# Kernel optimization log

Measured on AMD Instinct MI355X. Metric: run time of the kernel, lower is better.

## Reference

```python
import jax, jax.numpy as jnp
import numpy as np

GN_EPS = 1e-5
NUM_GROUPS = 32


def setup_inputs() -> dict:
    key = jax.random.key(0)
    ks = jax.random.split(key, 4)
    B, K, N = 8192, 2048, 4096
    bound = 1.0 / np.sqrt(K)
    return {
        "x": jax.random.normal(ks[0], (B, K), dtype=jnp.float32),
        "weight": jax.random.normal(ks[1], (N, K), dtype=jnp.float32) * bound,
        "bias_lin": jax.random.uniform(ks[2], (N,), dtype=jnp.float32, minval=-bound, maxval=bound),
        "bias_extra": jax.random.normal(ks[3], (N,), dtype=jnp.float32),
        "gn_weight": jnp.ones((N,), dtype=jnp.float32),
        "gn_bias": jnp.zeros((N,), dtype=jnp.float32),
    }


def reference(x, weight, bias_lin, bias_extra, gn_weight, gn_bias):
    # Fused GEMM + bias + Swish + extra bias:  y = swish(x @ W.T + b_lin) + b_ex
    z = jnp.einsum("bk,nk->bn", x, weight) + bias_lin          # [B, N]
    y = z * jax.nn.sigmoid(z) + bias_extra                      # Swish + extra bias
    # GroupNorm over channel groups
    B, N = y.shape
    G = NUM_GROUPS
    yg = y.reshape(B, G, N // G)
    mean = jnp.mean(yg, axis=2, keepdims=True)
    var = jnp.mean(jnp.square(yg - mean), axis=2, keepdims=True)  # biased variance
    y_norm = ((yg - mean) * jax.lax.rsqrt(var + GN_EPS)).reshape(B, N)
    return y_norm * gn_weight + gn_bias
```

## Files before the change

### kernel.cpp

```cpp
#include <hip/hip_runtime.h>


typedef __attribute__((ext_vector_type(8))) short short8;
typedef __attribute__((ext_vector_type(4))) float f32x4;

#define M_DIM 8192
#define N_DIM 4096
#define K_DIM 2048
#define BM 256
#define BN 256
#define BK 64
#define NT (K_DIM / BK)

__global__ void f32_to_bf16_k(const float* __restrict__ in, ushort* __restrict__ out, int n8) {
    int i = blockIdx.x * blockDim.x + threadIdx.x;
    if (i >= n8) return;
    const float4* p = (const float4*)in + 2 * (size_t)i;
    float4 a = p[0], b = p[1];
    float v[8] = {a.x, a.y, a.z, a.w, b.x, b.y, b.z, b.w};
    ushort rr[8];
#pragma unroll
    for (int j = 0; j < 8; ++j) {
        unsigned u = __float_as_uint(v[j]);
        rr[j] = (ushort)((u + 0x7fffu + ((u >> 16) & 1u)) >> 16);
    }
    uint4 o;
    o.x = (unsigned)rr[0] | ((unsigned)rr[1] << 16);
    o.y = (unsigned)rr[2] | ((unsigned)rr[3] << 16);
    o.z = (unsigned)rr[4] | ((unsigned)rr[5] << 16);
    o.w = (unsigned)rr[6] | ((unsigned)rr[7] << 16);
    ((uint4*)out)[i] = o;
}

__global__ __launch_bounds__(512, 2) void gemm_swish_gn(
    const ushort* __restrict__ xb, const ushort* __restrict__ wb,
    const float* __restrict__ bias_lin, const float* __restrict__ bias_extra,
    const float* __restrict__ gn_w, const float* __restrict__ gn_b,
    float* __restrict__ out)
{
    extern __shared__ __align__(16) ushort lds[];

    const int t = threadIdx.x;
    const int w = t >> 6;
    const int l = t & 63;
    const int wm = w >> 2;
    const int wn = w & 3;
    const int h = l >> 4;
    const int r = l & 15;

    const int bid = blockIdx.x;
    const int id = (bid & 7) * 64 + (bid >> 3);
    const int brow = id & 31;
    const int bcol = id >> 5;

    const int strow = t >> 3;
    const int scb = (t & 7) << 4;
    const int scbs = scb ^ ((strow & 7) << 4);
    const ushort* srcA[4];
    const ushort* srcB[4];
#pragma unroll
    for (int rd = 0; rd < 4; ++rd) {
        srcA[rd] = xb + (size_t)(brow * BM + rd * 64 + strow) * K_DIM + (scbs >> 1);
        srcB[rd] = wb + (size_t)(bcol * BN + rd * 64 + strow) * K_DIM + (scbs >> 1);
    }
    const int dstoff = t * 8;

#define STAGE(buf_) do {                                                          \
    _Pragma("unroll")                                                             \
    for (int rd = 0; rd < 4; ++rd) {                                              \
        __builtin_amdgcn_global_load_lds(                                         \
            (const __attribute__((address_space(1))) void*)srcA[rd],              \
            (__attribute__((address_space(3))) void*)&lds[((buf_)*2+0)*16384 + rd*4096 + dstoff], \
            16, 0, 0);                                                            \
        srcA[rd] += BK;                                                           \
    }                                                                             \
    _Pragma("unroll")                                                             \
    for (int rd = 0; rd < 4; ++rd) {                                              \
        __builtin_amdgcn_global_load_lds(                                         \
            (const __attribute__((address_space(1))) void*)srcB[rd],              \
            (__attribute__((address_space(3))) void*)&lds[((buf_)*2+1)*16384 + rd*4096 + dstoff], \
            16, 0, 0);                                                            \
        srcB[rd] += BK;                                                           \
    }                                                                             \
} while (0)

    f32x4 acc[8][4];
#pragma unroll
    for (int m = 0; m < 8; ++m)
#pragma unroll
        for (int n = 0; n < 4; ++n)
            acc[m][n] = f32x4{0.f, 0.f, 0.f, 0.f};

    STAGE(0);
    STAGE(1);

    const int xr = (r & 7) << 4;
    const int aBase = wm * 128 + r;
    const int bBase = wn * 64 + r;

    short8 aF[8], bF[8];

#pragma unroll 1
    for (int tt = 0; tt < NT; ++tt) {
        if (tt < NT - 1) asm volatile("s_waitcnt vmcnt(8)" ::: "memory");
        else             asm volatile("s_waitcnt vmcnt(0)" ::: "memory");
        __builtin_amdgcn_sched_barrier(0);
        __builtin_amdgcn_s_barrier();
        __builtin_amdgcn_sched_barrier(0);

        const int cur = tt & 1;
        const ushort* sA = &lds[(cur * 2 + 0) * 16384];
        const ushort* sB = &lds[(cur * 2 + 1) * 16384];

#pragma unroll
        for (int m = 0; m < 4; ++m)
#pragma unroll
            for (int kk = 0; kk < 2; ++kk) {
                int row = aBase + m * 16;
                aF[m * 2 + kk] = *(const short8*)&sA[(row * 128 + ((kk * 64 + h * 16) ^ xr)) >> 1];
            }
#pragma unroll
        for (int n = 0; n < 2; ++n)
#pragma unroll
            for (int kk = 0; kk < 2; ++kk) {
                int row = bBase + n * 16;
                bF[n * 2 + kk] = *(const short8*)&sB[(row * 128 + ((kk * 64 + h * 16) ^ xr)) >> 1];
            }
        __builtin_amdgcn_s_setprio(1);
#pragma unroll
        for (int m = 0; m < 4; ++m)
#pragma unroll
            for (int n = 0; n < 2; ++n)
#pragma unroll
                for (int kk = 0; kk < 2; ++kk)
                    acc[m][n] = __builtin_amdgcn_mfma_f32_16x16x32_bf16(aF[m * 2 + kk], bF[n * 2 + kk], acc[m][n], 0, 0, 0);
        __builtin_amdgcn_s_setprio(0);

#pragma unroll
        for (int n = 2; n < 4; ++n)
#pragma unroll
            for (int kk = 0; kk < 2; ++kk) {
                int row = bBase + n * 16;
                bF[n * 2 + kk] = *(const short8*)&sB[(row * 128 + ((kk * 64 + h * 16) ^ xr)) >> 1];
            }
        __builtin_amdgcn_s_setprio(1);
#pragma unroll
        for (int m = 0; m < 4; ++m)
#pragma unroll
            for (int n = 2; n < 4; ++n)
#pragma unroll
                for (int kk = 0; kk < 2; ++kk)
                    acc[m][n] = __builtin_amdgcn_mfma_f32_16x16x32_bf16(aF[m * 2 + kk], bF[n * 2 + kk], acc[m][n], 0, 0, 0);
        __builtin_amdgcn_s_setprio(0);

#pragma unroll
        for (int m = 4; m < 8; ++m)
#pragma unroll
            for (int kk = 0; kk < 2; ++kk) {
                int row = aBase + m * 16;
                aF[(m - 4) * 2 + kk] = *(const short8*)&sA[(row * 128 + ((kk * 64 + h * 16) ^ xr)) >> 1];
            }
        __builtin_amdgcn_s_setprio(1);
#pragma unroll
        for (int m = 4; m < 8; ++m)
#pragma unroll
            for (int n = 2; n < 4; ++n)
#pragma unroll
                for (int kk = 0; kk < 2; ++kk)
                    acc[m][n] = __builtin_amdgcn_mfma_f32_16x16x32_bf16(aF[(m - 4) * 2 + kk], bF[n * 2 + kk], acc[m][n], 0, 0, 0);
        __builtin_amdgcn_s_setprio(0);

        __builtin_amdgcn_s_barrier();
        if (tt + 2 < NT) STAGE(tt & 1);

        __builtin_amdgcn_s_setprio(1);
#pragma unroll
        for (int m = 4; m < 8; ++m)
#pragma unroll
            for (int n = 0; n < 2; ++n)
#pragma unroll
                for (int kk = 0; kk < 2; ++kk)
                    acc[m][n] = __builtin_amdgcn_mfma_f32_16x16x32_bf16(aF[(m - 4) * 2 + kk], bF[n * 2 + kk], acc[m][n], 0, 0, 0);
        __builtin_amdgcn_s_setprio(0);
    }

    const int colbase = bcol * BN + wn * 64;
    float bl[4], be[4], gwv[4], gbv[4];
#pragma unroll
    for (int n = 0; n < 4; ++n) {
        int col = colbase + n * 16 + r;
        bl[n] = bias_lin[col];
        be[n] = bias_extra[col];
        gwv[n] = gn_w[col];
        gbv[n] = gn_b[col];
    }

    float s1[8][4], s2[8][4];
#pragma unroll
    for (int m = 0; m < 8; ++m)
#pragma unroll
        for (int j = 0; j < 4; ++j) { s1[m][j] = 0.f; s2[m][j] = 0.f; }

#pragma unroll
    for (int m = 0; m < 8; ++m)
#pragma unroll
        for (int n = 0; n < 4; ++n)
#pragma unroll
            for (int j = 0; j < 4; ++j) {
                float z = acc[m][n][j] + bl[n];
                float sw = z / (1.f + __expf(-z)) + be[n];
                acc[m][n][j] = sw;
                s1[m][j] += sw;
                s2[m][j] += sw * sw;
            }

#pragma unroll
    for (int mask = 1; mask < 16; mask <<= 1) {
#pragma unroll
        for (int m = 0; m < 8; ++m)
#pragma unroll
            for (int j = 0; j < 4; ++j) {
                s1[m][j] += __shfl_xor(s1[m][j], mask, 16);
                s2[m][j] += __shfl_xor(s2[m][j], mask, 16);
            }
    }

    float* sred = (float*)lds;
    const int gh = wn >> 1;
    const int p = wn & 1;
    if (r == 0) {
#pragma unroll
        for (int m = 0; m < 8; ++m)
#pragma unroll
            for (int j = 0; j < 4; ++j) {
                int row = wm * 128 + m * 16 + h * 4 + j;
                sred[((0 * 2 + gh) * 2 + p) * 256 + row] = s1[m][j];
                sred[((1 * 2 + gh) * 2 + p) * 256 + row] = s2[m][j];
            }
    }
    __syncthreads();

    const size_t orow0 = (size_t)brow * BM;
#pragma unroll
    for (int m = 0; m < 8; ++m)
#pragma unroll
        for (int j = 0; j < 4; ++j) {
            int row = wm * 128 + m * 16 + h * 4 + j;
            float mu = (sred[((0 * 2 + gh) * 2 + 0) * 256 + row] +
                        sred[((0 * 2 + gh) * 2 + 1) * 256 + row]) * (1.f / 128.f);
            float ex2 = (sred[((1 * 2 + gh) * 2 + 0) * 256 + row] +
                         sred[((1 * 2 + gh) * 2 + 1) * 256 + row]) * (1.f / 128.f);
            float var = ex2 - mu * mu;
            float rs = rsqrtf(var + 1e-5f);
            float* orow = out + (orow0 + row) * N_DIM;
#pragma unroll
            for (int n = 0; n < 4; ++n) {
                int col = colbase + n * 16 + r;
                orow[col] = (acc[m][n][j] - mu) * rs * gwv[n] + gbv[n];
            }
        }
}

extern "C" void kernel_launch(void* const* d_in, const int* in_sizes, int n_in,
                              void* d_out, int out_size, void* d_ws, size_t ws_size,
                              hipStream_t stream) {
    const float* x        = (const float*)d_in[0];
    const float* weight   = (const float*)d_in[1];
    const float* bias_lin = (const float*)d_in[2];
    const float* bias_ex  = (const float*)d_in[3];
    const float* gn_w     = (const float*)d_in[4];
    const float* gn_b     = (const float*)d_in[5];
    float* out = (float*)d_out;

    ushort* xb = (ushort*)d_ws;
    ushort* wb = xb + (size_t)M_DIM * K_DIM;

    {
        int n8 = (M_DIM * K_DIM) / 8;
        f32_to_bf16_k<<<n8 / 256, 256, 0, stream>>>(x, xb, n8);
    }
    {
        int n8 = (N_DIM * K_DIM) / 8;
        f32_to_bf16_k<<<n8 / 256, 256, 0, stream>>>(weight, wb, n8);
    }

    static_assert(2 * 2 * 16384 * sizeof(ushort) == 131072, "lds size");
    (void)hipFuncSetAttribute((const void*)gemm_swish_gn,
                              hipFuncAttributeMaxDynamicSharedMemorySize, 131072);

    dim3 grid((M_DIM / BM) * (N_DIM / BN));
    gemm_swish_gn<<<grid, 512, 131072, stream>>>(xb, wb, bias_lin, bias_ex, gn_w, gn_b, out);
}
```

Before: 194.4 us.

## Restructure GEMM main loop into k32 half-steps with staggered A/B staging

Splits each BK=64 tile into two k=32 sub-steps, each held in its own LDS slot, and issues A and B global-to-LDS loads separately, interleaved between MFMA groups. Each barrier-separated phase can then overlap a smaller load with compute. The LDS layout changes from a 128-byte XOR-swizzled row to an unswizzled 64-byte row indexed directly. The goal is finer overlap of memory with MFMA work, at the cost of more barriers and lgkmcnt waits per tile. Dropping the swizzle also risks LDS bank conflicts on the fragment reads.

```diff
diff --git a/kernel.cpp b/kernel.cpp
--- a/kernel.cpp
+++ b/kernel.cpp
@@ -32,6 +32,11 @@
     ((uint4*)out)[i] = o;
 }
 
+
+#define BAR() __builtin_amdgcn_s_barrier()
+#define LGKM0() do { asm volatile("s_waitcnt lgkmcnt(0)" ::: "memory"); __builtin_amdgcn_sched_barrier(0); } while (0)
+#define VMC(n_) do { asm volatile("s_waitcnt vmcnt(" #n_ ")" ::: "memory"); __builtin_amdgcn_sched_barrier(0); } while (0)
+
 __global__ __launch_bounds__(512, 2) void gemm_swish_gn(
     const ushort* __restrict__ xb, const ushort* __restrict__ wb,
     const float* __restrict__ bias_lin, const float* __restrict__ bias_extra,
@@ -53,36 +58,32 @@
     const int brow = id & 31;
     const int bcol = id >> 5;
 
-    const int strow = t >> 3;
-    const int scb = (t & 7) << 4;
-    const int scbs = scb ^ ((strow & 7) << 4);
-    const ushort* srcA[4];
-    const ushort* srcB[4];
-#pragma unroll
-    for (int rd = 0; rd < 4; ++rd) {
-        srcA[rd] = xb + (size_t)(brow * BM + rd * 64 + strow) * K_DIM + (scbs >> 1);
-        srcB[rd] = wb + (size_t)(bcol * BN + rd * 64 + strow) * K_DIM + (scbs >> 1);
-    }
-    const int dstoff = t * 8;
-
-#define STAGE(buf_) do {                                                          \
-    _Pragma("unroll")                                                             \
-    for (int rd = 0; rd < 4; ++rd) {                                              \
-        __builtin_amdgcn_global_load_lds(                                         \
-            (const __attribute__((address_space(1))) void*)srcA[rd],              \
-            (__attribute__((address_space(3))) void*)&lds[((buf_)*2+0)*16384 + rd*4096 + dstoff], \
-            16, 0, 0);                                                            \
-        srcA[rd] += BK;                                                           \
-    }                                                                             \
-    _Pragma("unroll")                                                             \
-    for (int rd = 0; rd < 4; ++rd) {                                              \
-        __builtin_amdgcn_global_load_lds(                                         \
-            (const __attribute__((address_space(1))) void*)srcB[rd],              \
-            (__attribute__((address_space(3))) void*)&lds[((buf_)*2+1)*16384 + rd*4096 + dstoff], \
-            16, 0, 0);                                                            \
-        srcB[rd] += BK;                                                           \
-    }                                                                             \
-} while (0)
+    const ushort* pA0 = xb + (size_t)(brow * BM + (t >> 2)) * K_DIM + (t & 3) * 8;
+    const ushort* pA1 = pA0 + (size_t)128 * K_DIM;
+    const ushort* pB0 = wb + (size_t)(bcol * BN + (t >> 2)) * K_DIM + (t & 3) * 8;
+    const ushort* pB1 = pB0 + (size_t)128 * K_DIM;
+    const int dst0 = t * 8;
+
+#define STAGE_A(slotU) do {                                                   \
+    __builtin_amdgcn_global_load_lds(                                         \
+        (const __attribute__((address_space(1))) void*)pA0,                   \
+        (__attribute__((address_space(3))) void*)&lds[(slotU) + dst0], 16, 0, 0); \
+    __builtin_amdgcn_global_load_lds(                                         \
+        (const __attribute__((address_space(1))) void*)pA1,                   \
+        (__attribute__((address_space(3))) void*)&lds[(slotU) + 4096 + dst0], 16, 0, 0); \
+    pA0 += 32; pA1 += 32; } while (0)
+
+#define STAGE_B(slotU) do {                                                   \
+    __builtin_amdgcn_global_load_lds(                                         \
+        (const __attribute__((address_space(1))) void*)pB0,                   \
+        (__attribute__((address_space(3))) void*)&lds[(slotU) + dst0], 16, 0, 0); \
+    __builtin_amdgcn_global_load_lds(                                         \
+        (const __attribute__((address_space(1))) void*)pB1,                   \
+        (__attribute__((address_space(3))) void*)&lds[(slotU) + 4096 + dst0], 16, 0, 0); \
+    pB0 += 32; pB1 += 32; } while (0)
+
+    const int aIdx = (wm * 128 + r) * 32 + h * 8;
+    const int bIdx = (wn * 64 + r) * 32 + h * 8;
 
     f32x4 acc[8][4];
 #pragma unroll
@@ -91,97 +92,79 @@
         for (int n = 0; n < 4; ++n)
             acc[m][n] = f32x4{0.f, 0.f, 0.f, 0.f};
 
-    STAGE(0);
-    STAGE(1);
-
-    const int xr = (r & 7) << 4;
-    const int aBase = wm * 128 + r;
-    const int bBase = wn * 64 + r;
-
-    short8 aF[8], bF[8];
+    STAGE_A(0);
+    STAGE_B(16384);
+    STAGE_A(8192);
+    STAGE_B(24576);
+    STAGE_A(32768 + 0);
+    STAGE_B(32768 + 16384);
+    VMC(8);
+    BAR();
+
+    short8 aF[8], bF[4];
+
+#define DO_TILE(P, tt)                                                              \
+  {                                                                                 \
+                                                    \
+    _Pragma("unroll") for (int m = 0; m < 8; ++m)                                   \
+        aF[m] = *(const short8*)&lds[(P) * 32768 + aIdx + m * 512];                 \
+    bF[0] = *(const short8*)&lds[(P) * 32768 + 16384 + bIdx];                       \
+    bF[1] = *(const short8*)&lds[(P) * 32768 + 16384 + bIdx + 512];                 \
+    if ((tt) != NT - 1) STAGE_A(((P) ^ 1) * 32768 + 8192);                          \
+    BAR(); LGKM0();                                                                 \
+    __builtin_amdgcn_s_setprio(1);                                                  \
+    _Pragma("unroll") for (int m = 0; m < 8; ++m) {                                 \
+        acc[m][0] = __builtin_amdgcn_mfma_f32_16x16x32_bf16(aF[m], bF[0], acc[m][0], 0, 0, 0); \
+        acc[m][1] = __builtin_amdgcn_mfma_f32_16x16x32_bf16(aF[m], bF[1], acc[m][1], 0, 0, 0); \
+    }                                                                               \
+    __builtin_amdgcn_s_setprio(0);                                                  \
+    BAR();                                                                          \
+                                                    \
+    bF[2] = *(const short8*)&lds[(P) * 32768 + 16384 + bIdx + 1024];                \
+    bF[3] = *(const short8*)&lds[(P) * 32768 + 16384 + bIdx + 1536];                \
+    if ((tt) != NT - 1) STAGE_B(((P) ^ 1) * 32768 + 24576);                         \
+    BAR(); LGKM0();                                                                 \
+    __builtin_amdgcn_s_setprio(1);                                                  \
+    _Pragma("unroll") for (int m = 0; m < 8; ++m) {                                 \
+        acc[m][2] = __builtin_amdgcn_mfma_f32_16x16x32_bf16(aF[m], bF[2], acc[m][2], 0, 0, 0); \
+        acc[m][3] = __builtin_amdgcn_mfma_f32_16x16x32_bf16(aF[m], bF[3], acc[m][3], 0, 0, 0); \
+    }                                                                               \
+    __builtin_amdgcn_s_setprio(0);                                                  \
+    if ((tt) == NT - 1) { VMC(0); } else { VMC(8); }                                \
+    BAR();                                                                          \
+                                                    \
+    _Pragma("unroll") for (int m = 0; m < 8; ++m)                                   \
+        aF[m] = *(const short8*)&lds[(P) * 32768 + 8192 + aIdx + m * 512];          \
+    bF[0] = *(const short8*)&lds[(P) * 32768 + 24576 + bIdx];                       \
+    bF[1] = *(const short8*)&lds[(P) * 32768 + 24576 + bIdx + 512];                 \
+    if ((tt) < NT - 2) STAGE_A((P) * 32768 + 0);                                    \
+    BAR(); LGKM0();                                                                 \
+    __builtin_amdgcn_s_setprio(1);                                                  \
+    _Pragma("unroll") for (int m = 0; m < 8; ++m) {                                 \
+        acc[m][0] = __builtin_amdgcn_mfma_f32_16x16x32_bf16(aF[m], bF[0], acc[m][0], 0, 0, 0); \
+        acc[m][1] = __builtin_amdgcn_mfma_f32_16x16x32_bf16(aF[m], bF[1], acc[m][1], 0, 0, 0); \
+    }                                                                               \
+    __builtin_amdgcn_s_setprio(0);                                                  \
+    BAR();                                                                          \
+                                                    \
+    bF[2] = *(const short8*)&lds[(P) * 32768 + 24576 + bIdx + 1024];                \
+    bF[3] = *(const short8*)&lds[(P) * 32768 + 24576 + bIdx + 1536];                \
+    if ((tt) < NT - 2) STAGE_B((P) * 32768 + 16384);                                \
+    BAR(); LGKM0();                                                                 \
+    __builtin_amdgcn_s_setprio(1);                                                  \
+    _Pragma("unroll") for (int m = 0; m < 8; ++m) {                                 \
+        acc[m][2] = __builtin_amdgcn_mfma_f32_16x16x32_bf16(aF[m], bF[2], acc[m][2], 0, 0, 0); \
+        acc[m][3] = __builtin_amdgcn_mfma_f32_16x16x32_bf16(aF[m], bF[3], acc[m][3], 0, 0, 0); \
+    }                                                                               \
+    __builtin_amdgcn_s_setprio(0);                                                  \
+    if ((tt) == NT - 2) { VMC(4); } else if ((tt) < NT - 2) { VMC(8); }             \
+    BAR();                                                                          \
+  }
 
 #pragma unroll 1
-    for (int tt = 0; tt < NT; ++tt) {
-        if (tt < NT - 1) asm volatile("s_waitcnt vmcnt(8)" ::: "memory");
-        else             asm volatile("s_waitcnt vmcnt(0)" ::: "memory");
-        __builtin_amdgcn_sched_barrier(0);
-        __builtin_amdgcn_s_barrier();
-        __builtin_amdgcn_sched_barrier(0);
-
-        const int cur = tt & 1;
-        const ushort* sA = &lds[(cur * 2 + 0) * 16384];
-        const ushort* sB = &lds[(cur * 2 + 1) * 16384];
-
-#pragma unroll
-        for (int m = 0; m < 4; ++m)
-#pragma unroll
-            for (int kk = 0; kk < 2; ++kk) {
-                int row = aBase + m * 16;
-                aF[m * 2 + kk] = *(const short8*)&sA[(row * 128 + ((kk * 64 + h * 16) ^ xr)) >> 1];
-            }
-#pragma unroll
-        for (int n = 0; n < 2; ++n)
-#pragma unroll
-            for (int kk = 0; kk < 2; ++kk) {
-                int row = bBase + n * 16;
-                bF[n * 2 + kk] = *(const short8*)&sB[(row * 128 + ((kk * 64 + h * 16) ^ xr)) >> 1];
-            }
-        __builtin_amdgcn_s_setprio(1);
-#pragma unroll
-        for (int m = 0; m < 4; ++m)
-#pragma unroll
-            for (int n = 0; n < 2; ++n)
-#pragma unroll
-                for (int kk = 0; kk < 2; ++kk)
-                    acc[m][n] = __builtin_amdgcn_mfma_f32_16x16x32_bf16(aF[m * 2 + kk], bF[n * 2 + kk], acc[m][n], 0, 0, 0);
-        __builtin_amdgcn_s_setprio(0);
-
-#pragma unroll
-        for (int n = 2; n < 4; ++n)
-#pragma unroll
-            for (int kk = 0; kk < 2; ++kk) {
-                int row = bBase + n * 16;
-                bF[n * 2 + kk] = *(const short8*)&sB[(row * 128 + ((kk * 64 + h * 16) ^ xr)) >> 1];
-            }
-        __builtin_amdgcn_s_setprio(1);
-#pragma unroll
-        for (int m = 0; m < 4; ++m)
-#pragma unroll
-            for (int n = 2; n < 4; ++n)
-#pragma unroll
-                for (int kk = 0; kk < 2; ++kk)
-                    acc[m][n] = __builtin_amdgcn_mfma_f32_16x16x32_bf16(aF[m * 2 + kk], bF[n * 2 + kk], acc[m][n], 0, 0, 0);
-        __builtin_amdgcn_s_setprio(0);
-
-#pragma unroll
-        for (int m = 4; m < 8; ++m)
-#pragma unroll
-            for (int kk = 0; kk < 2; ++kk) {
-                int row = aBase + m * 16;
-                aF[(m - 4) * 2 + kk] = *(const short8*)&sA[(row * 128 + ((kk * 64 + h * 16) ^ xr)) >> 1];
-            }
-        __builtin_amdgcn_s_setprio(1);
-#pragma unroll
-        for (int m = 4; m < 8; ++m)
-#pragma unroll
-            for (int n = 2; n < 4; ++n)
-#pragma unroll
-                for (int kk = 0; kk < 2; ++kk)
-                    acc[m][n] = __builtin_amdgcn_mfma_f32_16x16x32_bf16(aF[(m - 4) * 2 + kk], bF[n * 2 + kk], acc[m][n], 0, 0, 0);
-        __builtin_amdgcn_s_setprio(0);
-
-        __builtin_amdgcn_s_barrier();
-        if (tt + 2 < NT) STAGE(tt & 1);
-
-        __builtin_amdgcn_s_setprio(1);
-#pragma unroll
-        for (int m = 4; m < 8; ++m)
-#pragma unroll
-            for (int n = 0; n < 2; ++n)
-#pragma unroll
-                for (int kk = 0; kk < 2; ++kk)
-                    acc[m][n] = __builtin_amdgcn_mfma_f32_16x16x32_bf16(aF[(m - 4) * 2 + kk], bF[n * 2 + kk], acc[m][n], 0, 0, 0);
-        __builtin_amdgcn_s_setprio(0);
+    for (int tp = 0; tp < NT; tp += 2) {
+        DO_TILE(0, tp);
+        DO_TILE(1, tp + 1);
     }
 
     const int colbase = bcol * BN + wn * 64;
@@ -284,7 +267,6 @@
         f32_to_bf16_k<<<n8 / 256, 256, 0, stream>>>(weight, wb, n8);
     }
 
-    static_assert(2 * 2 * 16384 * sizeof(ushort) == 131072, "lds size");
     (void)hipFuncSetAttribute((const void*)gemm_swish_gn,
                               hipFuncAttributeMaxDynamicSharedMemorySize, 131072);
 
```

After: 206.5 us. +6.2%, slower.
